# Kernel tuning notes

Hardware: AMD Instinct MI355X
Metric: run time of the kernel (lower is better)

Reference implementation:

```python
import jax, jax.numpy as jnp
import numpy as np

N, E, D = 50000, 600000, 128
BN_EPS = 1e-5


def setup_inputs() -> dict:
    key = jax.random.key(0)
    ks = jax.random.split(key, 16)
    lin = lambda k: (jax.random.normal(k, (D, D), jnp.float32) / np.sqrt(D),
                     jnp.zeros((D,), jnp.float32))
    Aw, Ab = lin(ks[0]); Bw, Bb = lin(ks[1]); Cw, Cb = lin(ks[2])
    Uw, Ub = lin(ks[3]); Vw, Vb = lin(ks[4])
    return {
        "h": jax.random.normal(ks[5], (N, D), jnp.float32),
        "e": jax.random.normal(ks[6], (E, D), jnp.float32),
        "senders": jax.random.randint(ks[7], (E,), 0, N, jnp.int32),
        "receivers": jax.random.randint(ks[8], (E,), 0, N, jnp.int32),
        "Aw": Aw, "Ab": Ab, "Bw": Bw, "Bb": Bb, "Cw": Cw, "Cb": Cb,
        "Uw": Uw, "Ub": Ub, "Vw": Vw, "Vb": Vb,
        "bn_e_scale": jnp.ones((D,), jnp.float32),
        "bn_e_offset": jnp.zeros((D,), jnp.float32),
        "bn_n_scale": jnp.ones((D,), jnp.float32),
        "bn_n_offset": jnp.zeros((D,), jnp.float32),
    }


def _batch_norm(x, scale, offset):
    # training-mode BN over the leading (edge/node) axis
    mean = jnp.mean(x, axis=0)
    var = jnp.var(x, axis=0)
    return (x - mean) * jax.lax.rsqrt(var + BN_EPS) * scale + offset


def reference(h, e, senders, receivers, Aw, Ab, Bw, Bb, Cw, Cb,
              Uw, Ub, Vw, Vb, bn_e_scale, bn_e_offset, bn_n_scale, bn_n_offset):
    n_nodes = h.shape[0]
    h_i = h[senders]      # [E, D] gather
    h_j = h[receivers]    # [E, D] gather
    # edge logits eta = A(h_i) + B(h_j) + C(e)
    eta = (h_i @ Aw + Ab) + (h_j @ Bw + Bb) + (e @ Cw + Cb)
    e_feat = jax.nn.relu(_batch_norm(eta, bn_e_scale, bn_e_offset))
    e_new = e + e_feat  # residual
    # weight_on_edges=True -> gate from updated edge features
    w_sigma = jax.nn.sigmoid(e_new)
    w_sigma_sum = jax.ops.segment_sum(w_sigma, senders, num_segments=n_nodes) + 1e-6
    unattnd = (h_j @ Vw + Vb) * w_sigma
    agg = jax.ops.segment_sum(unattnd, senders, num_segments=n_nodes)
    node_feat = (h @ Uw + Ub) + agg / w_sigma_sum
    node_feat = jax.nn.relu(_batch_norm(node_feat, bn_n_scale, bn_n_offset))
    h_new = h + node_feat  # residual (dropout rate 0.0 -> identity)
    return h_new, e_new
```

## Files before the change

### kernel.cpp

```cpp
#include <hip/hip_runtime.h>

#define D 128

using short8 = __attribute__((ext_vector_type(8))) short;
using f32x4  = __attribute__((ext_vector_type(4))) float;

__device__ __forceinline__ unsigned short f2bf(float f) {
    unsigned int u = __builtin_bit_cast(unsigned int, f);
    unsigned int r = (u + 0x7fffu + ((u >> 16) & 1u)) >> 16;
    return (unsigned short)r;
}

__device__ __forceinline__ short8 pack8(f32x4 a, f32x4 b) {
    short8 r;
    r[0] = (short)f2bf(a[0]); r[1] = (short)f2bf(a[1]);
    r[2] = (short)f2bf(a[2]); r[3] = (short)f2bf(a[3]);
    r[4] = (short)f2bf(b[0]); r[5] = (short)f2bf(b[1]);
    r[6] = (short)f2bf(b[2]); r[7] = (short)f2bf(b[3]);
    return r;
}

__global__ void __launch_bounds__(256) prep_frags(
    const float* __restrict__ Aw, const float* __restrict__ Bw,
    const float* __restrict__ Cw, const float* __restrict__ Uw,
    const float* __restrict__ Vw,
    unsigned short* __restrict__ BfragC, unsigned short* __restrict__ BfragN)
{
    int t = blockIdx.x * 256 + threadIdx.x;
    if (t < 2048) {
        int lane = t & 63;
        int slot = t >> 6;
        int kc = slot & 3, ct = slot >> 2;
        int n  = ct * 16 + (lane & 15);
        int kb = kc * 32 + (lane >> 4) * 8;
        #pragma unroll
        for (int i = 0; i < 8; ++i)
            BfragC[t * 8 + i] = f2bf(Cw[(kb + i) * D + n]);
    } else if (t < 2048 + 8192) {
        int u = t - 2048;
        int lane = u & 63;
        int slot = u >> 6;
        int kc = slot & 3, ct = (slot >> 2) & 15, cg = slot >> 6;
        int n512 = cg * 256 + ct * 16 + (lane & 15);
        int m = n512 >> 7, d = n512 & 127;
        const float* W = (m == 0) ? Aw : (m == 1) ? Bw : (m == 2) ? Vw : Uw;
        int kb = kc * 32 + (lane >> 4) * 8;
        #pragma unroll
        for (int i = 0; i < 8; ++i)
            BfragN[u * 8 + i] = f2bf(W[(kb + i) * D + d]);
    }
}

__global__ void __launch_bounds__(256) node_gemm(
    const float* __restrict__ h, const unsigned short* __restrict__ BfragN,
    const float* __restrict__ Ab, const float* __restrict__ Bb,
    const float* __restrict__ Vb, const float* __restrict__ Ub,
    float* __restrict__ hA, float* __restrict__ hB,
    float* __restrict__ hV, float* __restrict__ hU, int N)
{
    __shared__ unsigned short lbf[32768];
    const int tid = threadIdx.x, lane = tid & 63, wave = tid >> 6;
    const int cg = blockIdx.y;
    {
        const f32x4* src = (const f32x4*)(BfragN + (size_t)cg * 32768);
        f32x4* dst = (f32x4*)lbf;
        for (int i = tid; i < 4096; i += 256) dst[i] = src[i];
    }
    const int rowWave = blockIdx.x * 256 + wave * 64;
    short8 afr[4][4];
    #pragma unroll
    for (int rt = 0; rt < 4; ++rt) {
        int row = rowWave + rt * 16 + (lane & 15);
        row = min(row, N - 1);
        const float* hp = h + (size_t)row * D + (lane >> 4) * 8;
        #pragma unroll
        for (int kc = 0; kc < 4; ++kc) {
            f32x4 x0 = *(const f32x4*)(hp + kc * 32);
            f32x4 x1 = *(const f32x4*)(hp + kc * 32 + 4);
            afr[rt][kc] = pack8(x0, x1);
        }
    }
    __syncthreads();
    #pragma unroll 1
    for (int ct = 0; ct < 16; ++ct) {
        f32x4 acc[4];
        #pragma unroll
        for (int rt = 0; rt < 4; ++rt) acc[rt] = (f32x4){0.f, 0.f, 0.f, 0.f};
        #pragma unroll
        for (int kc = 0; kc < 4; ++kc) {
            short8 bfr = *(const short8*)(lbf + ((size_t)(ct * 4 + kc) * 64 + lane) * 8);
            #pragma unroll
            for (int rt = 0; rt < 4; ++rt)
                acc[rt] = __builtin_amdgcn_mfma_f32_16x16x32_bf16(afr[rt][kc], bfr, acc[rt], 0, 0, 0);
        }
        int n512 = cg * 256 + ct * 16 + (lane & 15);
        int m = n512 >> 7, d = n512 & 127;
        const float* bias = (m == 0) ? Ab : (m == 1) ? Bb : (m == 2) ? Vb : Ub;
        float* dstp       = (m == 0) ? hA : (m == 1) ? hB : (m == 2) ? hV : hU;
        float bv = bias[d];
        #pragma unroll
        for (int rt = 0; rt < 4; ++rt) {
            int rbase = rowWave + rt * 16 + ((lane >> 4) * 4);
            #pragma unroll
            for (int j = 0; j < 4; ++j) {
                int row = rbase + j;
                if (row < N) dstp[(size_t)row * D + d] = acc[rt][j] + bv;
            }
        }
    }
}

__global__ void __launch_bounds__(256) edge_gemm(
    const float* __restrict__ e, const int* __restrict__ senders,
    const int* __restrict__ receivers, const unsigned short* __restrict__ BfragC,
    const float* __restrict__ Cb, const float* __restrict__ hA,
    const float* __restrict__ hB, float* __restrict__ etaout,
    float* __restrict__ estats, int E)
{
    __shared__ unsigned short lbf[16384];
    __shared__ float lstats[4][256];
    const int tid = threadIdx.x, lane = tid & 63, wave = tid >> 6;
    {
        const f32x4* src = (const f32x4*)BfragC;
        f32x4* dst = (f32x4*)lbf;
        for (int i = tid; i < 2048; i += 256) dst[i] = src[i];
    }
    for (int i = lane; i < 256; i += 64) lstats[wave][i] = 0.f;
    const int ebase = blockIdx.x * 256 + wave * 64;
    short8 afr[4][4];
    #pragma unroll
    for (int rt = 0; rt < 4; ++rt) {
        int row = ebase + rt * 16 + (lane & 15);
        row = min(row, E - 1);
        const float* ep = e + (size_t)row * D + (lane >> 4) * 8;
        #pragma unroll
        for (int kc = 0; kc < 4; ++kc) {
            f32x4 x0 = *(const f32x4*)(ep + kc * 32);
            f32x4 x1 = *(const f32x4*)(ep + kc * 32 + 4);
            afr[rt][kc] = pack8(x0, x1);
        }
    }
    int sidx[4][4], ridx[4][4];
    #pragma unroll
    for (int rt = 0; rt < 4; ++rt) {
        #pragma unroll
        for (int j = 0; j < 4; ++j) {
            int ed = ebase + rt * 16 + ((lane >> 4) * 4) + j;
            int ec = min(ed, E - 1);
            sidx[rt][j] = senders[ec];
            ridx[rt][j] = receivers[ec];
        }
    }
    __syncthreads();
    #pragma unroll 1
    for (int ct = 0; ct < 8; ++ct) {
        f32x4 acc[4];
        #pragma unroll
        for (int rt = 0; rt < 4; ++rt) acc[rt] = (f32x4){0.f, 0.f, 0.f, 0.f};
        #pragma unroll
        for (int kc = 0; kc < 4; ++kc) {
            short8 bfr = *(const short8*)(lbf + ((size_t)(ct * 4 + kc) * 64 + lane) * 8);
            #pragma unroll
            for (int rt = 0; rt < 4; ++rt)
                acc[rt] = __builtin_amdgcn_mfma_f32_16x16x32_bf16(afr[rt][kc], bfr, acc[rt], 0, 0, 0);
        }
        int col = ct * 16 + (lane & 15);
        float cb = Cb[col];
        float ps = 0.f, ps2 = 0.f;
        #pragma unroll
        for (int rt = 0; rt < 4; ++rt) {
            int rbase = ebase + rt * 16 + ((lane >> 4) * 4);
            #pragma unroll
            for (int j = 0; j < 4; ++j) {
                int ed = rbase + j;
                if (ed < E) {
                    float v = acc[rt][j] + cb
                            + hA[(size_t)sidx[rt][j] * D + col]
                            + hB[(size_t)ridx[rt][j] * D + col];
                    etaout[(size_t)ed * D + col] = v;
                    ps  += v;
                    ps2 += v * v;
                }
            }
        }
        ps  += __shfl_xor(ps, 16);  ps  += __shfl_xor(ps, 32);
        ps2 += __shfl_xor(ps2, 16); ps2 += __shfl_xor(ps2, 32);
        if (lane < 16) {
            lstats[wave][col]       += ps;
            lstats[wave][128 + col] += ps2;
        }
    }
    __syncthreads();
    float v = lstats[0][tid] + lstats[1][tid] + lstats[2][tid] + lstats[3][tid];
    unsafeAtomicAdd(&estats[(blockIdx.x & 31) * 256 + tid], v);
}

__global__ void finalize_stats(const float* __restrict__ stats,
    const float* __restrict__ scale, const float* __restrict__ offset,
    float* __restrict__ scsh, float cnt)
{
    int c = threadIdx.x;
    if (c >= 128) return;
    float s = 0.f, s2 = 0.f;
    for (int b = 0; b < 32; ++b) { s += stats[b * 256 + c]; s2 += stats[b * 256 + 128 + c]; }
    float mean = s / cnt;
    float var  = fmaxf(s2 / cnt - mean * mean, 0.f);
    float rs   = rsqrtf(var + 1e-5f);
    float sc   = scale[c] * rs;
    scsh[c]       = sc;
    scsh[128 + c] = offset[c] - mean * sc;
}

__global__ void __launch_bounds__(256) edge_bn_kernel(
    const float* __restrict__ e, const float* __restrict__ scsh,
    float* __restrict__ e_out, int total4)
{
    int idx = blockIdx.x * 256 + threadIdx.x;
    if (idx >= total4) return;
    size_t off = (size_t)idx * 4;
    int c0 = (int)(off & 127);
    f32x4 ev = *(const f32x4*)(e + off);
    f32x4 et = *(const f32x4*)(e_out + off);
    f32x4 sc = *(const f32x4*)(scsh + c0);
    f32x4 sh = *(const f32x4*)(scsh + 128 + c0);
    f32x4 en;
    #pragma unroll
    for (int k = 0; k < 4; ++k) {
        float f = fmaxf(et[k] * sc[k] + sh[k], 0.f);
        en[k] = ev[k] + f;
    }
    *(f32x4*)(e_out + off) = en;
}

__global__ void __launch_bounds__(256) csr_hist(
    const int* __restrict__ senders, int* __restrict__ counts, int E)
{
    int i = blockIdx.x * 256 + threadIdx.x;
    if (i < E) atomicAdd(&counts[senders[i]], 1);
}

__global__ void __launch_bounds__(1024) csr_scan(
    const int* __restrict__ counts, int* __restrict__ rowstart,
    int* __restrict__ cursor, int N)
{
    __shared__ int psum[1024];
    int tid = threadIdx.x;
    int chunk = (N + 1023) / 1024;
    int lo = tid * chunk, hi = min(lo + chunk, N);
    if (lo > N) lo = N;
    if (hi < lo) hi = lo;
    int s = 0;
    for (int i = lo; i < hi; ++i) s += counts[i];
    psum[tid] = s;
    __syncthreads();
    for (int off = 1; off < 1024; off <<= 1) {
        int v = (tid >= off) ? psum[tid - off] : 0;
        __syncthreads();
        psum[tid] += v;
        __syncthreads();
    }
    int base = (tid == 0) ? 0 : psum[tid - 1];
    for (int i = lo; i < hi; ++i) {
        rowstart[i] = base;
        cursor[i]   = base;
        base += counts[i];
    }
    if (tid == 1023) rowstart[N] = psum[1023];
}

__global__ void __launch_bounds__(256) csr_fill(
    const int* __restrict__ senders, int* __restrict__ cursor,
    int* __restrict__ elist, int E)
{
    int i = blockIdx.x * 256 + threadIdx.x;
    if (i < E) {
        int pos = atomicAdd(&cursor[senders[i]], 1);
        elist[pos] = i;
    }
}

__global__ void __launch_bounds__(256) node_agg_kernel(
    const float* __restrict__ e_new, const int* __restrict__ receivers,
    const int* __restrict__ rowstart, const int* __restrict__ elist,
    const float* __restrict__ hV, const float* __restrict__ hU,
    float* __restrict__ nf, float* __restrict__ nstats, int N)
{
    __shared__ float lsum[128], lsq[128];
    const int half = threadIdx.x >> 7;
    const int c    = threadIdx.x & 127;
    const int n    = blockIdx.x * 2 + half;
    float v = 0.f;
    if (n < N) {
        float w = 0.f, a = 0.f;
        int lo = rowstart[n], hi = rowstart[n + 1];
        for (int k = lo; k < hi; ++k) {
            int eidx = elist[k];
            int r    = receivers[eidx];
            float ev = e_new[(size_t)eidx * D + c];
            float sw = 1.f / (1.f + __expf(-ev));
            a += hV[(size_t)r * D + c] * sw;
            w += sw;
        }
        v = hU[(size_t)n * D + c] + a / (w + 1e-6f);
        nf[(size_t)n * D + c] = v;
    }
    if (half == 0) { lsum[c] = v;  lsq[c] = v * v; }
    __syncthreads();
    if (half == 1) { lsum[c] += v; lsq[c] += v * v; }
    __syncthreads();
    if (half == 0) {
        float* sb = nstats + (blockIdx.x & 31) * 256;
        unsafeAtomicAdd(sb + c, lsum[c]);
        unsafeAtomicAdd(sb + 128 + c, lsq[c]);
    }
}

__global__ void __launch_bounds__(256) node_out_kernel(
    const float* __restrict__ h, const float* __restrict__ nf,
    const float* __restrict__ scsh, float* __restrict__ out, int N)
{
    int idx = blockIdx.x * 256 + threadIdx.x;
    if (idx >= N * 32) return;
    size_t i4 = (size_t)idx * 4;
    int c0 = (int)(i4 & 127);
    f32x4 hh = *(const f32x4*)(h + i4);
    f32x4 v  = *(const f32x4*)(nf + i4);
    f32x4 sc = *(const f32x4*)(scsh + c0);
    f32x4 sh = *(const f32x4*)(scsh + 128 + c0);
    f32x4 o;
    #pragma unroll
    for (int k = 0; k < 4; ++k) {
        float f = fmaxf(v[k] * sc[k] + sh[k], 0.f);
        o[k] = hh[k] + f;
    }
    *(f32x4*)(out + i4) = o;
}

extern "C" void kernel_launch(void* const* d_in, const int* in_sizes, int n_in,
                              void* d_out, int out_size, void* d_ws, size_t ws_size,
                              hipStream_t stream)
{
    const float* h  = (const float*)d_in[0];
    const float* e  = (const float*)d_in[1];
    const int* senders   = (const int*)d_in[2];
    const int* receivers = (const int*)d_in[3];
    const float* Aw = (const float*)d_in[4];
    const float* Ab = (const float*)d_in[5];
    const float* Bw = (const float*)d_in[6];
    const float* Bb = (const float*)d_in[7];
    const float* Cw = (const float*)d_in[8];
    const float* Cb = (const float*)d_in[9];
    const float* Uw = (const float*)d_in[10];
    const float* Ub = (const float*)d_in[11];
    const float* Vw = (const float*)d_in[12];
    const float* Vb = (const float*)d_in[13];
    const float* bnEs = (const float*)d_in[14];
    const float* bnEo = (const float*)d_in[15];
    const float* bnNs = (const float*)d_in[16];
    const float* bnNo = (const float*)d_in[17];

    const int N = in_sizes[0] / D;
    const int E = in_sizes[1] / D;

    float* out   = (float*)d_out;
    float* out_h = out;
    float* out_e = out + (size_t)N * D;

    float* ws     = (float*)d_ws;
    float* hA     = ws;
    float* hB     = hA + (size_t)N * D;
    float* hV     = hB + (size_t)N * D;
    float* hU     = hV + (size_t)N * D;
    float* estats = hU + (size_t)N * D;
    float* nstats = estats + 32 * 256;
    float* scsh_e = nstats + 32 * 256;
    float* scsh_n = scsh_e + 256;
    int* counts   = (int*)(scsh_n + 256);
    int* rowstart = counts + N;
    int* cursor   = rowstart + N + 1;
    int* elist    = cursor + N;
    unsigned short* BfragC = (unsigned short*)(elist + E);
    unsigned short* BfragN = BfragC + 16384;
    float* nf = hA;

    hipMemsetAsync(estats, 0, (size_t)(2 * 32 * 256 + 2 * 256 + N) * sizeof(float), stream);

    prep_frags<<<40, 256, 0, stream>>>(Aw, Bw, Cw, Uw, Vw, BfragC, BfragN);

    csr_hist<<<(E + 255) / 256, 256, 0, stream>>>(senders, counts, E);
    csr_scan<<<1, 1024, 0, stream>>>(counts, rowstart, cursor, N);
    csr_fill<<<(E + 255) / 256, 256, 0, stream>>>(senders, cursor, elist, E);

    dim3 g1((N + 255) / 256, 2);
    node_gemm<<<g1, 256, 0, stream>>>(h, BfragN, Ab, Bb, Vb, Ub, hA, hB, hV, hU, N);

    edge_gemm<<<(E + 255) / 256, 256, 0, stream>>>(e, senders, receivers, BfragC, Cb,
                                                   hA, hB, out_e, estats, E);
    finalize_stats<<<1, 128, 0, stream>>>(estats, bnEs, bnEo, scsh_e, (float)E);

    edge_bn_kernel<<<(E * 32 + 255) / 256, 256, 0, stream>>>(e, scsh_e, out_e, E * 32);

    node_agg_kernel<<<(N + 1) / 2, 256, 0, stream>>>(out_e, receivers, rowstart, elist,
                                                     hV, hU, nf, nstats, N);
    finalize_stats<<<1, 128, 0, stream>>>(nstats, bnNs, bnNo, scsh_n, (float)N);
    node_out_kernel<<<(N * 32 + 255) / 256, 256, 0, stream>>>(h, nf, scsh_n, out_h, N);
}
```

Measured before the change: 1.423 ms.

## Store gathered node projections in bf16 and unroll aggregation loop

The node projections hA, hB and hV are now written as bf16 tables, which halves the bytes moved by the random gathers in edge_gemm and node_agg. hU stays fp32 and nf gets its own buffer. The edge-stats LDS reduction is replaced by direct per-column atomics on each ct iteration. The node aggregation loop is unrolled by two so more independent loads are in flight. The cost is extra rounding error in eta and agg, and more atomic traffic.

```diff
diff --git a/kernel.cpp b/kernel.cpp
--- a/kernel.cpp
+++ b/kernel.cpp
@@ -9,6 +9,11 @@
     unsigned int u = __builtin_bit_cast(unsigned int, f);
     unsigned int r = (u + 0x7fffu + ((u >> 16) & 1u)) >> 16;
     return (unsigned short)r;
+}
+
+__device__ __forceinline__ float bf2f(unsigned short u) {
+    unsigned int x = ((unsigned int)u) << 16;
+    return __builtin_bit_cast(float, x);
 }
 
 __device__ __forceinline__ short8 pack8(f32x4 a, f32x4 b) {
@@ -55,8 +60,8 @@
     const float* __restrict__ h, const unsigned short* __restrict__ BfragN,
     const float* __restrict__ Ab, const float* __restrict__ Bb,
     const float* __restrict__ Vb, const float* __restrict__ Ub,
-    float* __restrict__ hA, float* __restrict__ hB,
-    float* __restrict__ hV, float* __restrict__ hU, int N)
+    unsigned short* __restrict__ hAb, unsigned short* __restrict__ hBb,
+    unsigned short* __restrict__ hVb, float* __restrict__ hU, int N)
 {
     __shared__ unsigned short lbf[32768];
     const int tid = threadIdx.x, lane = tid & 63, wave = tid >> 6;
@@ -96,15 +101,19 @@
         int n512 = cg * 256 + ct * 16 + (lane & 15);
         int m = n512 >> 7, d = n512 & 127;
         const float* bias = (m == 0) ? Ab : (m == 1) ? Bb : (m == 2) ? Vb : Ub;
-        float* dstp       = (m == 0) ? hA : (m == 1) ? hB : (m == 2) ? hV : hU;
         float bv = bias[d];
+        unsigned short* tbl = (m == 0) ? hAb : (m == 1) ? hBb : hVb;
         #pragma unroll
         for (int rt = 0; rt < 4; ++rt) {
             int rbase = rowWave + rt * 16 + ((lane >> 4) * 4);
             #pragma unroll
             for (int j = 0; j < 4; ++j) {
                 int row = rbase + j;
-                if (row < N) dstp[(size_t)row * D + d] = acc[rt][j] + bv;
+                if (row < N) {
+                    float val = acc[rt][j] + bv;
+                    if (m < 3) tbl[(size_t)row * D + d] = f2bf(val);
+                    else       hU[(size_t)row * D + d] = val;
+                }
             }
         }
     }
@@ -113,20 +122,18 @@
 __global__ void __launch_bounds__(256) edge_gemm(
     const float* __restrict__ e, const int* __restrict__ senders,
     const int* __restrict__ receivers, const unsigned short* __restrict__ BfragC,
-    const float* __restrict__ Cb, const float* __restrict__ hA,
-    const float* __restrict__ hB, float* __restrict__ etaout,
+    const float* __restrict__ Cb, const unsigned short* __restrict__ hAb,
+    const unsigned short* __restrict__ hBb, float* __restrict__ etaout,
     float* __restrict__ estats, int E)
 {
     __shared__ unsigned short lbf[16384];
-    __shared__ float lstats[4][256];
-    const int tid = threadIdx.x, lane = tid & 63, wave = tid >> 6;
+    const int tid = threadIdx.x, lane = tid & 63;
     {
         const f32x4* src = (const f32x4*)BfragC;
         f32x4* dst = (f32x4*)lbf;
         for (int i = tid; i < 2048; i += 256) dst[i] = src[i];
     }
-    for (int i = lane; i < 256; i += 64) lstats[wave][i] = 0.f;
-    const int ebase = blockIdx.x * 256 + wave * 64;
+    const int ebase = blockIdx.x * 256 + (tid >> 6) * 64;
     short8 afr[4][4];
     #pragma unroll
     for (int rt = 0; rt < 4; ++rt) {
@@ -152,6 +159,7 @@
         }
     }
     __syncthreads();
+    float* sb = estats + (blockIdx.x & 31) * 256;
     #pragma unroll 1
     for (int ct = 0; ct < 8; ++ct) {
         f32x4 acc[4];
@@ -175,8 +183,8 @@
                 int ed = rbase + j;
                 if (ed < E) {
                     float v = acc[rt][j] + cb
-                            + hA[(size_t)sidx[rt][j] * D + col]
-                            + hB[(size_t)ridx[rt][j] * D + col];
+                            + bf2f(hAb[(size_t)sidx[rt][j] * D + col])
+                            + bf2f(hBb[(size_t)ridx[rt][j] * D + col]);
                     etaout[(size_t)ed * D + col] = v;
                     ps  += v;
                     ps2 += v * v;
@@ -186,13 +194,10 @@
         ps  += __shfl_xor(ps, 16);  ps  += __shfl_xor(ps, 32);
         ps2 += __shfl_xor(ps2, 16); ps2 += __shfl_xor(ps2, 32);
         if (lane < 16) {
-            lstats[wave][col]       += ps;
-            lstats[wave][128 + col] += ps2;
-        }
-    }
-    __syncthreads();
-    float v = lstats[0][tid] + lstats[1][tid] + lstats[2][tid] + lstats[3][tid];
-    unsafeAtomicAdd(&estats[(blockIdx.x & 31) * 256 + tid], v);
+            unsafeAtomicAdd(sb + col, ps);
+            unsafeAtomicAdd(sb + 128 + col, ps2);
+        }
+    }
 }
 
 __global__ void finalize_stats(const float* __restrict__ stats,
@@ -282,7 +287,7 @@
 __global__ void __launch_bounds__(256) node_agg_kernel(
     const float* __restrict__ e_new, const int* __restrict__ receivers,
     const int* __restrict__ rowstart, const int* __restrict__ elist,
-    const float* __restrict__ hV, const float* __restrict__ hU,
+    const unsigned short* __restrict__ hVb, const float* __restrict__ hU,
     float* __restrict__ nf, float* __restrict__ nstats, int N)
 {
     __shared__ float lsum[128], lsq[128];
@@ -293,13 +298,26 @@
     if (n < N) {
         float w = 0.f, a = 0.f;
         int lo = rowstart[n], hi = rowstart[n + 1];
-        for (int k = lo; k < hi; ++k) {
-            int eidx = elist[k];
-            int r    = receivers[eidx];
-            float ev = e_new[(size_t)eidx * D + c];
-            float sw = 1.f / (1.f + __expf(-ev));
-            a += hV[(size_t)r * D + c] * sw;
-            w += sw;
+        int k = lo;
+        for (; k + 1 < hi; k += 2) {
+            int e0 = elist[k], e1 = elist[k + 1];
+            int r0 = receivers[e0], r1 = receivers[e1];
+            float ev0 = e_new[(size_t)e0 * D + c];
+            float ev1 = e_new[(size_t)e1 * D + c];
+            float hv0 = bf2f(hVb[(size_t)r0 * D + c]);
+            float hv1 = bf2f(hVb[(size_t)r1 * D + c]);
+            float s0 = 1.f / (1.f + __expf(-ev0));
+            float s1 = 1.f / (1.f + __expf(-ev1));
+            a += hv0 * s0 + hv1 * s1;
+            w += s0 + s1;
+        }
+        if (k < hi) {
+            int e0 = elist[k];
+            int r0 = receivers[e0];
+            float ev0 = e_new[(size_t)e0 * D + c];
+            float s0 = 1.f / (1.f + __expf(-ev0));
+            a += bf2f(hVb[(size_t)r0 * D + c]) * s0;
+            w += s0;
         }
         v = hU[(size_t)n * D + c] + a / (w + 1e-6f);
         nf[(size_t)n * D + c] = v;
@@ -367,11 +385,9 @@
     float* out_e = out + (size_t)N * D;
 
     float* ws     = (float*)d_ws;
-    float* hA     = ws;
-    float* hB     = hA + (size_t)N * D;
-    float* hV     = hB + (size_t)N * D;
-    float* hU     = hV + (size_t)N * D;
-    float* estats = hU + (size_t)N * D;
+    float* hU     = ws;
+    float* nf     = hU + (size_t)N * D;
+    float* estats = nf + (size_t)N * D;
     float* nstats = estats + 32 * 256;
     float* scsh_e = nstats + 32 * 256;
     float* scsh_n = scsh_e + 256;
@@ -379,9 +395,11 @@
     int* rowstart = counts + N;
     int* cursor   = rowstart + N + 1;
     int* elist    = cursor + N;
-    unsigned short* BfragC = (unsigned short*)(elist + E);
+    unsigned short* hAb = (unsigned short*)(elist + E);
+    unsigned short* hBb = hAb + (size_t)N * D;
+    unsigned short* hVb = hBb + (size_t)N * D;
+    unsigned short* BfragC = hVb + (size_t)N * D;
     unsigned short* BfragN = BfragC + 16384;
-    float* nf = hA;
 
     hipMemsetAsync(estats, 0, (size_t)(2 * 32 * 256 + 2 * 256 + N) * sizeof(float), stream);
 
@@ -392,16 +410,16 @@
     csr_fill<<<(E + 255) / 256, 256, 0, stream>>>(senders, cursor, elist, E);
 
     dim3 g1((N + 255) / 256, 2);
-    node_gemm<<<g1, 256, 0, stream>>>(h, BfragN, Ab, Bb, Vb, Ub, hA, hB, hV, hU, N);
+    node_gemm<<<g1, 256, 0, stream>>>(h, BfragN, Ab, Bb, Vb, Ub, hAb, hBb, hVb, hU, N);
 
     edge_gemm<<<(E + 255) / 256, 256, 0, stream>>>(e, senders, receivers, BfragC, Cb,
-                                                   hA, hB, out_e, estats, E);
+                                                   hAb, hBb, out_e, estats, E);
     finalize_stats<<<1, 128, 0, stream>>>(estats, bnEs, bnEo, scsh_e, (float)E);
 
     edge_bn_kernel<<<(E * 32 + 255) / 256, 256, 0, stream>>>(e, scsh_e, out_e, E * 32);
 
     node_agg_kernel<<<(N + 1) / 2, 256, 0, stream>>>(out_e, receivers, rowstart, elist,
-                                                     hV, hU, nf, nstats, N);
+                                                     hVb, hU, nf, nstats, N);
     finalize_stats<<<1, 128, 0, stream>>>(nstats, bnNs, bnNo, scsh_n, (float)N);
     node_out_kernel<<<(N * 32 + 255) / 256, 256, 0, stream>>>(h, nf, scsh_n, out_h, N);
 }
```

Result: faster. 1.355 ms (-4.8%).
